# Kernel tuning notes

Hardware: AMD Instinct MI355X
Metric: run time of the kernel (lower is better)

## Reference

```python
import jax, jax.numpy as jnp
import numpy as np

D_MODEL = 1024
N_HEADS = 16
HEAD_DIM = D_MODEL // N_HEADS


def setup_inputs() -> dict:
    key = jax.random.key(0)
    ks = jax.random.split(key, 9)
    B, T = 2, 2048
    s = 1.0 / np.sqrt(D_MODEL)
    inp = {
        "x": jax.random.normal(ks[0], (B, T, D_MODEL), dtype=jnp.float32),
        "w_q": jax.random.normal(ks[1], (D_MODEL, D_MODEL), dtype=jnp.float32) * s,
        "b_q": jnp.zeros((D_MODEL,), dtype=jnp.float32),
        "w_k": jax.random.normal(ks[2], (D_MODEL, D_MODEL), dtype=jnp.float32) * s,
        "b_k": jnp.zeros((D_MODEL,), dtype=jnp.float32),
        "w_v": jax.random.normal(ks[3], (D_MODEL, D_MODEL), dtype=jnp.float32) * s,
        "b_v": jnp.zeros((D_MODEL,), dtype=jnp.float32),
        "w_o": jax.random.normal(ks[4], (D_MODEL, D_MODEL), dtype=jnp.float32) * s,
        "b_o": jnp.zeros((D_MODEL,), dtype=jnp.float32),
    }
    return inp


def reference(x, w_q, b_q, w_k, b_k, w_v, b_v, w_o, b_o):
    B, T, C = x.shape
    H, Dh = N_HEADS, HEAD_DIM
    # projections (weights stored as [out,in] like torch Linear -> x @ W.T + b)
    q = (x @ w_q.T + b_q).reshape(B, T, H, Dh).transpose(0, 2, 1, 3)  # [B,H,T,Dh]
    k = (x @ w_k.T + b_k).reshape(B, T, H, Dh).transpose(0, 2, 1, 3)
    v = (x @ w_v.T + b_v).reshape(B, T, H, Dh).transpose(0, 2, 1, 3)
    scale = 1.0 / jnp.sqrt(jnp.asarray(Dh, dtype=x.dtype))
    scores = jnp.einsum("bhqd,bhkd->bhqk", q, k) * scale  # [B,H,T,T]
    causal = jnp.tril(jnp.ones((T, T), dtype=bool))
    scores = jnp.where(causal[None, None], scores, jnp.asarray(-jnp.inf, dtype=scores.dtype))
    attn = jax.nn.softmax(scores, axis=-1)
    out = jnp.einsum("bhqk,bhkd->bhqd", attn, v)  # [B,H,T,Dh]
    out = out.transpose(0, 2, 1, 3).reshape(B, T, C)
    return out @ w_o.T + b_o
```

## Files before the change

### kernel.cpp

```cpp
#include <hip/hip_runtime.h>
#include <hip/hip_bf16.h>
#include <math.h>

#define BATCH 2
#define SEQ   2048
#define DMODEL 1024
#define NHEADS 16
#define HDIM  64
#define MROWS (BATCH*SEQ)
#define QSCALE 0.1803368801111204f

typedef __attribute__((ext_vector_type(8))) short bfr8;
typedef __attribute__((ext_vector_type(4))) float f32x4;

__device__ inline unsigned short f2bf(float f) {
    union { float f; unsigned u; } v; v.f = f;
    unsigned r = v.u + 0x7FFFu + ((v.u >> 16) & 1u);
    return (unsigned short)(r >> 16);
}

__device__ inline unsigned pack2bf(float a, float b) {
    union { __hip_bfloat162 h; unsigned u; } cv;
    cv.h = __float22bfloat162_rn(float2{a, b});
    return cv.u;
}

__device__ inline void gload16(const unsigned short* g, unsigned short* l) {
    __builtin_amdgcn_global_load_lds((const __attribute__((address_space(1))) void*)g,
        (__attribute__((address_space(3))) void*)l, 16, 0, 0);
}

__global__ __launch_bounds__(256) void cast_bf16(const float* __restrict__ in,
                                                 unsigned short* __restrict__ out, int n) {
    int i = (blockIdx.x * 256 + threadIdx.x) * 4;
    const int stride = gridDim.x * 256 * 4;
    for (; i < n; i += stride) {
        float4 v = *(const float4*)(in + i);
        ushort4 o;
        o.x = f2bf(v.x); o.y = f2bf(v.y); o.z = f2bf(v.z); o.w = f2bf(v.w);
        *(ushort4*)(out + i) = o;
    }
}

__global__ __launch_bounds__(256) void cast4_bf16(
    const float* __restrict__ a, const float* __restrict__ b,
    const float* __restrict__ c, const float* __restrict__ d,
    unsigned short* __restrict__ out) {
    const int NW = 1 << 20;
    int i = (blockIdx.x * 256 + threadIdx.x) * 4;
    const int stride = gridDim.x * 256 * 4;
    for (; i < 4 * NW; i += stride) {
        const int seg = i >> 20;
        const float* src = seg == 0 ? a : seg == 1 ? b : seg == 2 ? c : d;
        float4 v = *(const float4*)(src + (i & (NW - 1)));
        ushort4 o;
        o.x = f2bf(v.x); o.y = f2bf(v.y); o.z = f2bf(v.z); o.w = f2bf(v.w);
        *(ushort4*)(out + i) = o;
    }
}

template<int BM, int MODE>
__global__ __launch_bounds__(256) void gemm_bf16(
    const unsigned short* __restrict__ A, const unsigned short* __restrict__ W,
    const float* __restrict__ b0, const float* __restrict__ b1,
    const float* __restrict__ b2, void* __restrict__ Y)
{
    __shared__ __align__(16) unsigned short As[2][4][BM][8];
    __shared__ __align__(16) unsigned short Bs[2][4][128][8];

    const int tid = threadIdx.x;
    const int l = tid & 63, w = tid >> 6;
    const int wr = w >> 1, wc = w & 1;
    const int m0 = blockIdx.y * BM, n0 = blockIdx.x * 128;
    const int r15 = l & 15, g = l >> 4;
    constexpr int MR = BM / 32;

    f32x4 acc[MR][4] = {};

    auto stage = [&](int buf, int k0) {
        #pragma unroll
        for (int s = 0; s < BM / 64; ++s) {
            int idx = s * 256 + tid;
            int row = idx % BM, kg = idx / BM;
            gload16(A + (size_t)(m0 + row) * 1024 + k0 + kg * 8, &As[buf][kg][row][0]);
        }
        #pragma unroll
        for (int s = 0; s < 2; ++s) {
            int idx = s * 256 + tid;
            int row = idx & 127, kg = idx >> 7;
            gload16(W + (size_t)(n0 + row) * 1024 + k0 + kg * 8, &Bs[buf][kg][row][0]);
        }
    };

    stage(0, 0);
    __syncthreads();

    for (int t = 0; t < 32; ++t) {
        const int buf = t & 1;
        if (t + 1 < 32) stage(buf ^ 1, (t + 1) * 32);
        bfr8 a[MR], b[4];
        #pragma unroll
        for (int m = 0; m < MR; ++m)
            a[m] = *(const bfr8*)&As[buf][g][wr * (BM / 2) + m * 16 + r15][0];
        #pragma unroll
        for (int n = 0; n < 4; ++n)
            b[n] = *(const bfr8*)&Bs[buf][g][wc * 64 + n * 16 + r15][0];
        #pragma unroll
        for (int m = 0; m < MR; ++m)
            #pragma unroll
            for (int n = 0; n < 4; ++n)
                acc[m][n] = __builtin_amdgcn_mfma_f32_16x16x32_bf16(a[m], b[n], acc[m][n], 0, 0, 0);
        __syncthreads();
    }

    const size_t NX = (size_t)MROWS * DMODEL;
    #pragma unroll
    for (int m = 0; m < MR; ++m) {
        const int rowb = m0 + wr * (BM / 2) + m * 16 + g * 4;
        #pragma unroll
        for (int n = 0; n < 4; ++n) {
            const int col = n0 + wc * 64 + n * 16 + r15;
            const int proj = col >> 10, within = col & 1023;
            const float bc = (MODE == 2) ? b0[col]
                           : (proj == 0 ? b0[within] : proj == 1 ? b1[within] : b2[within]);
            #pragma unroll
            for (int i = 0; i < 4; ++i) {
                float v = acc[m][n][i] + bc;
                const int rr = rowb + i;
                if (MODE == 2) {
                    ((float*)Y)[(size_t)rr * 1024 + col] = v;
                } else {
                    if (proj == 0) v *= QSCALE;
                    const int bb = rr >> 11, tt = rr & 2047;
                    const int hh = within >> 6, dd = within & 63;
                    unsigned short* dst = (unsigned short*)Y + (size_t)proj * NX;
                    size_t idx;
                    if (proj < 2)
                        idx = (((size_t)bb * NHEADS + hh) * SEQ + tt) * HDIM + dd;
                    else
                        idx = (((size_t)bb * NHEADS + hh) * HDIM + dd) * SEQ + tt;
                    dst[idx] = f2bf(v);
                }
            }
        }
    }
}

__global__ __launch_bounds__(256, 2) void attn_mfma(
    const unsigned short* __restrict__ Q, const unsigned short* __restrict__ K,
    const unsigned short* __restrict__ VT, unsigned short* __restrict__ O)
{
    __shared__ __align__(16) unsigned short Ks[2][64][64];
    __shared__ __align__(16) unsigned short Vs[2][64][64];
    __shared__ __align__(16) unsigned short Ps[4][2][16][8][8];

    const int tid = threadIdx.x;
    const int l = tid & 63, w = tid >> 6;
    const int r15 = l & 15, g2 = (l >> 4) & 3;
    const int q0 = SEQ - 128 - blockIdx.x * 128;
    const int qw = q0 + w * 32;
    const int bh = blockIdx.y;

    const unsigned short* Qb = Q + (size_t)bh * SEQ * HDIM;
    const unsigned short* Kb = K + (size_t)bh * SEQ * HDIM;
    const unsigned short* Vb = VT + (size_t)bh * HDIM * SEQ;

    bfr8 qf[2][2];
    #pragma unroll
    for (int rf = 0; rf < 2; ++rf)
        #pragma unroll
        for (int ks = 0; ks < 2; ++ks)
            qf[rf][ks] = *(const bfr8*)(Qb + (size_t)(qw + rf * 16 + r15) * HDIM + ks * 32 + g2 * 8);

    auto stage = [&](int buf, int kv0) {
        #pragma unroll
        for (int s = 0; s < 2; ++s) {
            int idx = s * 256 + tid;
            int row = idx >> 3, gs = idx & 7;
            gload16(Kb + (size_t)(kv0 + row) * HDIM + ((gs ^ (row & 7)) * 8), &Ks[buf][row][gs * 8]);
            gload16(Vb + (size_t)row * SEQ + kv0 + ((gs ^ (row & 7)) * 8), &Vs[buf][row][gs * 8]);
        }
    };

    f32x4 o[4][2] = {};
    float mrow[2] = {-INFINITY, -INFINITY}, lrow[2] = {0.f, 0.f};

    const int ntiles = q0 / 64 + 2;
    stage(0, 0);
    __syncthreads();

    for (int kt = 0; kt < ntiles; ++kt) {
        const int kv0 = kt * 64, buf = kt & 1;
        if (kt + 1 < ntiles) stage(buf ^ 1, kv0 + 64);

        f32x4 s[4][2];
        #pragma unroll
        for (int c = 0; c < 4; ++c) {
            const int rk = c * 16 + r15;
            const bfr8 kf0 = *(const bfr8*)&Ks[buf][rk][(g2 ^ (r15 & 7)) * 8];
            const bfr8 kf1 = *(const bfr8*)&Ks[buf][rk][((4 + g2) ^ (r15 & 7)) * 8];
            #pragma unroll
            for (int rf = 0; rf < 2; ++rf) {
                f32x4 z = {0.f, 0.f, 0.f, 0.f};
                z = __builtin_amdgcn_mfma_f32_16x16x32_bf16(kf0, qf[rf][0], z, 0, 0, 0);
                s[c][rf] = __builtin_amdgcn_mfma_f32_16x16x32_bf16(kf1, qf[rf][1], z, 0, 0, 0);
            }
        }

        if (kt >= ntiles - 2) {
            #pragma unroll
            for (int c = 0; c < 4; ++c)
                #pragma unroll
                for (int rf = 0; rf < 2; ++rf) {
                    const int q = qw + rf * 16 + r15;
                    #pragma unroll
                    for (int i = 0; i < 4; ++i)
                        if (kv0 + c * 16 + g2 * 4 + i > q) s[c][rf][i] = -INFINITY;
                }
        }

        float scl[2];
        #pragma unroll
        for (int rf = 0; rf < 2; ++rf) {
            float tm = s[0][rf][0];
            #pragma unroll
            for (int c = 0; c < 4; ++c)
                #pragma unroll
                for (int i = 0; i < 4; ++i) tm = fmaxf(tm, s[c][rf][i]);
            tm = fmaxf(tm, __shfl_xor(tm, 16));
            tm = fmaxf(tm, __shfl_xor(tm, 32));
            const float mn = fmaxf(mrow[rf], tm);
            scl[rf] = exp2f(mrow[rf] - mn);
            mrow[rf] = mn;
            float ls = 0.f;
            #pragma unroll
            for (int c = 0; c < 4; ++c)
                #pragma unroll
                for (int i = 0; i < 4; ++i) {
                    const float p = exp2f(s[c][rf][i] - mn);
                    s[c][rf][i] = p;
                    ls += p;
                }
            ls += __shfl_xor(ls, 16);
            ls += __shfl_xor(ls, 32);
            lrow[rf] = lrow[rf] * scl[rf] + ls;
            #pragma unroll
            for (int c = 0; c < 4; ++c) {
                const int kgw = (c * 2 + (g2 >> 1)) ^ (r15 & 7);
                #pragma unroll
                for (int p = 0; p < 2; ++p) {
                    unsigned pk = pack2bf(s[c][rf][2 * p], s[c][rf][2 * p + 1]);
                    *(unsigned*)&Ps[w][rf][r15][kgw][(g2 & 1) * 4 + 2 * p] = pk;
                }
            }
        }

        #pragma unroll
        for (int rf = 0; rf < 2; ++rf) {
            float sb[4];
            #pragma unroll
            for (int i = 0; i < 4; ++i) sb[i] = __shfl(scl[rf], g2 * 4 + i, 16);
            #pragma unroll
            for (int ch = 0; ch < 4; ++ch)
                #pragma unroll
                for (int i = 0; i < 4; ++i) o[ch][rf][i] *= sb[i];
        }
        bfr8 pf[2][2];
        #pragma unroll
        for (int rf = 0; rf < 2; ++rf)
            #pragma unroll
            for (int ks = 0; ks < 2; ++ks)
                pf[rf][ks] = *(const bfr8*)&Ps[w][rf][r15][(ks * 4 + g2) ^ (r15 & 7)][0];
        #pragma unroll
        for (int ch = 0; ch < 4; ++ch) {
            const int d = ch * 16 + r15;
            const bfr8 vf0 = *(const bfr8*)&Vs[buf][d][(g2 ^ (r15 & 7)) * 8];
            const bfr8 vf1 = *(const bfr8*)&Vs[buf][d][((4 + g2) ^ (r15 & 7)) * 8];
            #pragma unroll
            for (int rf = 0; rf < 2; ++rf) {
                o[ch][rf] = __builtin_amdgcn_mfma_f32_16x16x32_bf16(pf[rf][0], vf0, o[ch][rf], 0, 0, 0);
                o[ch][rf] = __builtin_amdgcn_mfma_f32_16x16x32_bf16(pf[rf][1], vf1, o[ch][rf], 0, 0, 0);
            }
        }
        __syncthreads();
    }

    const int b = bh >> 4, h = bh & 15;
    #pragma unroll
    for (int rf = 0; rf < 2; ++rf) {
        const float inv = 1.f / lrow[rf];
        float ib[4];
        #pragma unroll
        for (int i = 0; i < 4; ++i) ib[i] = __shfl(inv, g2 * 4 + i, 16);
        #pragma unroll
        for (int i = 0; i < 4; ++i) {
            const int row = qw + rf * 16 + g2 * 4 + i;
            #pragma unroll
            for (int ch = 0; ch < 4; ++ch) {
                const int col = h * HDIM + ch * 16 + r15;
                O[((size_t)b * SEQ + row) * DMODEL + col] = f2bf(o[ch][rf][i] * ib[i]);
            }
        }
    }
}

extern "C" void kernel_launch(void* const* d_in, const int* in_sizes, int n_in,
                              void* d_out, int out_size, void* d_ws, size_t ws_size,
                              hipStream_t stream) {
    const float* x   = (const float*)d_in[0];
    const float* w_q = (const float*)d_in[1];
    const float* b_q = (const float*)d_in[2];
    const float* w_k = (const float*)d_in[3];
    const float* b_k = (const float*)d_in[4];
    const float* w_v = (const float*)d_in[5];
    const float* b_v = (const float*)d_in[6];
    const float* w_o = (const float*)d_in[7];
    const float* b_o = (const float*)d_in[8];
    float* out = (float*)d_out;

    const size_t NX = (size_t)MROWS * DMODEL;
    const size_t NW = (size_t)DMODEL * DMODEL;
    unsigned short* xb    = (unsigned short*)d_ws;
    unsigned short* wcomb = xb + NX;
    unsigned short* wob   = wcomb + 3 * NW;
    unsigned short* Qw    = wob + NW;
    unsigned short* Kw    = Qw + NX;
    unsigned short* VTw   = Kw + NX;
    unsigned short* Ow    = VTw + NX;

    cast_bf16<<<1024, 256, 0, stream>>>(x, xb, (int)NX);
    cast4_bf16<<<2048, 256, 0, stream>>>(w_q, w_k, w_v, w_o, wcomb);

    gemm_bf16<128, 0><<<dim3(24, 32), 256, 0, stream>>>(xb, wcomb, b_q, b_k, b_v, Qw);

    attn_mfma<<<dim3(16, 32), 256, 0, stream>>>(Qw, Kw, VTw, Ow);

    gemm_bf16<64, 2><<<dim3(8, 64), 256, 0, stream>>>(Ow, wob, b_o, nullptr, nullptr, out);
}
```

Baseline: 190.9 us.

## Shrink attention tile to 64 queries, swap PV MFMA operands, lazy softmax rescale

The attention kernel now gives each block 64 query rows (16 per wave) instead of 128. This doubles the grid and allows 4 blocks per CU through the launch bound. Query tiles are staggered across heads to spread the causal workload, and the PV MFMA takes V as the first operand so O lands with rows per lane. That removes the per-row scale shuffles and allows packed 8-byte output stores. The softmax max rescale is skipped unless the max grows by more than 8 in log2 units, which saves multiplies on O but relies on bounded fp32 headroom and adds K/V reloads per query row.

Result: faster. 160.8 us (-15.7%).

```diff
diff --git a/kernel.cpp b/kernel.cpp
--- a/kernel.cpp
+++ b/kernel.cpp
@@ -146,31 +146,29 @@
     }
 }
 
-__global__ __launch_bounds__(256, 2) void attn_mfma(
+__global__ __launch_bounds__(256, 4) void attn_mfma(
     const unsigned short* __restrict__ Q, const unsigned short* __restrict__ K,
     const unsigned short* __restrict__ VT, unsigned short* __restrict__ O)
 {
     __shared__ __align__(16) unsigned short Ks[2][64][64];
     __shared__ __align__(16) unsigned short Vs[2][64][64];
-    __shared__ __align__(16) unsigned short Ps[4][2][16][8][8];
+    __shared__ __align__(16) unsigned short Ps[4][8][16][8];
 
     const int tid = threadIdx.x;
     const int l = tid & 63, w = tid >> 6;
-    const int r15 = l & 15, g2 = (l >> 4) & 3;
-    const int q0 = SEQ - 128 - blockIdx.x * 128;
-    const int qw = q0 + w * 32;
+    const int r15 = l & 15, g2 = l >> 4;
+    const int qt = (blockIdx.x + blockIdx.y) & 31;
+    const int q0 = SEQ - 64 - qt * 64;
+    const int q  = q0 + w * 16 + r15;
     const int bh = blockIdx.y;
 
     const unsigned short* Qb = Q + (size_t)bh * SEQ * HDIM;
     const unsigned short* Kb = K + (size_t)bh * SEQ * HDIM;
     const unsigned short* Vb = VT + (size_t)bh * HDIM * SEQ;
 
-    bfr8 qf[2][2];
-    #pragma unroll
-    for (int rf = 0; rf < 2; ++rf)
-        #pragma unroll
-        for (int ks = 0; ks < 2; ++ks)
-            qf[rf][ks] = *(const bfr8*)(Qb + (size_t)(qw + rf * 16 + r15) * HDIM + ks * 32 + g2 * 8);
+    bfr8 qf[2];
+    qf[0] = *(const bfr8*)(Qb + (size_t)q * HDIM + g2 * 8);
+    qf[1] = *(const bfr8*)(Qb + (size_t)q * HDIM + 32 + g2 * 8);
 
     auto stage = [&](int buf, int kv0) {
         #pragma unroll
@@ -182,10 +180,10 @@
         }
     };
 
-    f32x4 o[4][2] = {};
-    float mrow[2] = {-INFINITY, -INFINITY}, lrow[2] = {0.f, 0.f};
-
-    const int ntiles = q0 / 64 + 2;
+    f32x4 o[4] = {};
+    float m = -INFINITY, rden = 0.f;
+
+    const int ntiles = q0 / 64 + 1;
     stage(0, 0);
     __syncthreads();
 
@@ -193,114 +191,88 @@
         const int kv0 = kt * 64, buf = kt & 1;
         if (kt + 1 < ntiles) stage(buf ^ 1, kv0 + 64);
 
-        f32x4 s[4][2];
+        f32x4 s[4];
         #pragma unroll
         for (int c = 0; c < 4; ++c) {
             const int rk = c * 16 + r15;
             const bfr8 kf0 = *(const bfr8*)&Ks[buf][rk][(g2 ^ (r15 & 7)) * 8];
             const bfr8 kf1 = *(const bfr8*)&Ks[buf][rk][((4 + g2) ^ (r15 & 7)) * 8];
-            #pragma unroll
-            for (int rf = 0; rf < 2; ++rf) {
-                f32x4 z = {0.f, 0.f, 0.f, 0.f};
-                z = __builtin_amdgcn_mfma_f32_16x16x32_bf16(kf0, qf[rf][0], z, 0, 0, 0);
-                s[c][rf] = __builtin_amdgcn_mfma_f32_16x16x32_bf16(kf1, qf[rf][1], z, 0, 0, 0);
-            }
-        }
-
-        if (kt >= ntiles - 2) {
+            f32x4 z = {0.f, 0.f, 0.f, 0.f};
+            z = __builtin_amdgcn_mfma_f32_16x16x32_bf16(kf0, qf[0], z, 0, 0, 0);
+            s[c] = __builtin_amdgcn_mfma_f32_16x16x32_bf16(kf1, qf[1], z, 0, 0, 0);
+        }
+
+        if (kt == ntiles - 1) {
             #pragma unroll
             for (int c = 0; c < 4; ++c)
                 #pragma unroll
-                for (int rf = 0; rf < 2; ++rf) {
-                    const int q = qw + rf * 16 + r15;
-                    #pragma unroll
-                    for (int i = 0; i < 4; ++i)
-                        if (kv0 + c * 16 + g2 * 4 + i > q) s[c][rf][i] = -INFINITY;
-                }
-        }
-
-        float scl[2];
-        #pragma unroll
-        for (int rf = 0; rf < 2; ++rf) {
-            float tm = s[0][rf][0];
-            #pragma unroll
-            for (int c = 0; c < 4; ++c)
-                #pragma unroll
-                for (int i = 0; i < 4; ++i) tm = fmaxf(tm, s[c][rf][i]);
-            tm = fmaxf(tm, __shfl_xor(tm, 16));
-            tm = fmaxf(tm, __shfl_xor(tm, 32));
-            const float mn = fmaxf(mrow[rf], tm);
-            scl[rf] = exp2f(mrow[rf] - mn);
-            mrow[rf] = mn;
-            float ls = 0.f;
-            #pragma unroll
-            for (int c = 0; c < 4; ++c)
-                #pragma unroll
-                for (int i = 0; i < 4; ++i) {
-                    const float p = exp2f(s[c][rf][i] - mn);
-                    s[c][rf][i] = p;
-                    ls += p;
-                }
-            ls += __shfl_xor(ls, 16);
-            ls += __shfl_xor(ls, 32);
-            lrow[rf] = lrow[rf] * scl[rf] + ls;
-            #pragma unroll
-            for (int c = 0; c < 4; ++c) {
-                const int kgw = (c * 2 + (g2 >> 1)) ^ (r15 & 7);
-                #pragma unroll
-                for (int p = 0; p < 2; ++p) {
-                    unsigned pk = pack2bf(s[c][rf][2 * p], s[c][rf][2 * p + 1]);
-                    *(unsigned*)&Ps[w][rf][r15][kgw][(g2 & 1) * 4 + 2 * p] = pk;
-                }
-            }
-        }
-
-        #pragma unroll
-        for (int rf = 0; rf < 2; ++rf) {
-            float sb[4];
-            #pragma unroll
-            for (int i = 0; i < 4; ++i) sb[i] = __shfl(scl[rf], g2 * 4 + i, 16);
+                for (int i = 0; i < 4; ++i)
+                    if (kv0 + c * 16 + g2 * 4 + i > q) s[c][i] = -INFINITY;
+        }
+
+        float tm = s[0][0];
+        #pragma unroll
+        for (int c = 0; c < 4; ++c)
+            #pragma unroll
+            for (int i = 0; i < 4; ++i) tm = fmaxf(tm, s[c][i]);
+        tm = fmaxf(tm, __shfl_xor(tm, 16));
+        tm = fmaxf(tm, __shfl_xor(tm, 32));
+        if (__any(tm > m + 8.f)) {
+            const float mn = fmaxf(m, tm);
+            const float scl = exp2f(m - mn);
+            m = mn;
+            rden *= scl;
             #pragma unroll
             for (int ch = 0; ch < 4; ++ch)
                 #pragma unroll
-                for (int i = 0; i < 4; ++i) o[ch][rf][i] *= sb[i];
-        }
-        bfr8 pf[2][2];
-        #pragma unroll
-        for (int rf = 0; rf < 2; ++rf)
-            #pragma unroll
-            for (int ks = 0; ks < 2; ++ks)
-                pf[rf][ks] = *(const bfr8*)&Ps[w][rf][r15][(ks * 4 + g2) ^ (r15 & 7)][0];
+                for (int i = 0; i < 4; ++i) o[ch][i] *= scl;
+        }
+        float ls = 0.f;
+        #pragma unroll
+        for (int c = 0; c < 4; ++c)
+            #pragma unroll
+            for (int i = 0; i < 4; ++i) {
+                const float p = exp2f(s[c][i] - m);
+                s[c][i] = p;
+                ls += p;
+            }
+        ls += __shfl_xor(ls, 16);
+        ls += __shfl_xor(ls, 32);
+        rden += ls;
+
+        {
+            const int eb = (g2 & 1) * 4;
+            #pragma unroll
+            for (int c = 0; c < 4; ++c) {
+                const int kg = c * 2 + (g2 >> 1);
+                *(unsigned*)&Ps[w][kg][r15][eb]     = pack2bf(s[c][0], s[c][1]);
+                *(unsigned*)&Ps[w][kg][r15][eb + 2] = pack2bf(s[c][2], s[c][3]);
+            }
+        }
+        bfr8 pf[2];
+        pf[0] = *(const bfr8*)&Ps[w][g2][r15][0];
+        pf[1] = *(const bfr8*)&Ps[w][4 + g2][r15][0];
+
         #pragma unroll
         for (int ch = 0; ch < 4; ++ch) {
             const int d = ch * 16 + r15;
             const bfr8 vf0 = *(const bfr8*)&Vs[buf][d][(g2 ^ (r15 & 7)) * 8];
             const bfr8 vf1 = *(const bfr8*)&Vs[buf][d][((4 + g2) ^ (r15 & 7)) * 8];
-            #pragma unroll
-            for (int rf = 0; rf < 2; ++rf) {
-                o[ch][rf] = __builtin_amdgcn_mfma_f32_16x16x32_bf16(pf[rf][0], vf0, o[ch][rf], 0, 0, 0);
-                o[ch][rf] = __builtin_amdgcn_mfma_f32_16x16x32_bf16(pf[rf][1], vf1, o[ch][rf], 0, 0, 0);
-            }
+            o[ch] = __builtin_amdgcn_mfma_f32_16x16x32_bf16(vf0, pf[0], o[ch], 0, 0, 0);
+            o[ch] = __builtin_amdgcn_mfma_f32_16x16x32_bf16(vf1, pf[1], o[ch], 0, 0, 0);
         }
         __syncthreads();
     }
 
+    const float inv = 1.f / rden;
     const int b = bh >> 4, h = bh & 15;
+    unsigned short* Ob = O + ((size_t)b * SEQ + q) * DMODEL + h * HDIM + g2 * 4;
     #pragma unroll
-    for (int rf = 0; rf < 2; ++rf) {
-        const float inv = 1.f / lrow[rf];
-        float ib[4];
-        #pragma unroll
-        for (int i = 0; i < 4; ++i) ib[i] = __shfl(inv, g2 * 4 + i, 16);
-        #pragma unroll
-        for (int i = 0; i < 4; ++i) {
-            const int row = qw + rf * 16 + g2 * 4 + i;
-            #pragma unroll
-            for (int ch = 0; ch < 4; ++ch) {
-                const int col = h * HDIM + ch * 16 + r15;
-                O[((size_t)b * SEQ + row) * DMODEL + col] = f2bf(o[ch][rf][i] * ib[i]);
-            }
-        }
+    for (int ch = 0; ch < 4; ++ch) {
+        uint2 pk;
+        pk.x = pack2bf(o[ch][0] * inv, o[ch][1] * inv);
+        pk.y = pack2bf(o[ch][2] * inv, o[ch][3] * inv);
+        *(uint2*)(Ob + ch * 16) = pk;
     }
 }
 
@@ -333,7 +305,7 @@
 
     gemm_bf16<128, 0><<<dim3(24, 32), 256, 0, stream>>>(xb, wcomb, b_q, b_k, b_v, Qw);
 
-    attn_mfma<<<dim3(16, 32), 256, 0, stream>>>(Qw, Kw, VTw, Ow);
+    attn_mfma<<<dim3(32, 32), 256, 0, stream>>>(Qw, Kw, VTw, Ow);
 
     gemm_bf16<64, 2><<<dim3(8, 64), 256, 0, stream>>>(Ow, wob, b_o, nullptr, nullptr, out);
 }
```
